# Optimization experiments

Hardware: AMD Instinct MI355X
Metric: run time of the kernel (lower is better)

Reference implementation:

```python
import jax, jax.numpy as jnp
import numpy as np
import math

C = 256
HEADS = 8
WS1 = (8, 8)
SS1 = (0, 0)
WS2 = (8, 8)
SS2 = (4, 4)
CPB_HIDDEN = 512


def _rel_pos_index(ws):
    coords = np.stack(np.meshgrid(np.arange(ws[0]), np.arange(ws[1]), indexing="ij")).reshape(2, -1)
    rel = (coords[:, :, None] - coords[:, None, :]).transpose(1, 2, 0).astype(np.int64)
    rel[..., 0] += ws[0] - 1
    rel[..., 1] += ws[1] - 1
    rel[..., 0] *= 2 * ws[1] - 1
    return rel.sum(-1).reshape(-1)


def _coords_table(ws):
    ch = np.arange(-(ws[0] - 1), ws[0], dtype=np.float32)
    cw = np.arange(-(ws[1] - 1), ws[1], dtype=np.float32)
    t = np.stack(np.meshgrid(ch, cw, indexing="ij"), axis=-1)
    t[..., 0] /= ws[0] - 1
    t[..., 1] /= ws[1] - 1
    t *= 8.0
    t = np.sign(t) * np.log2(np.abs(t) + 1.0) / 3.0
    return t.reshape(-1, 2)


def _swin_mask(pH, pW, ws, ss):
    # standard swin shifted-window attention mask, [num_windows, N, N]
    m = np.zeros((pH, pW), dtype=np.float32)
    cnt = 0.0
    hs = ((0, pH - ws[0]), (pH - ws[0], pH - ss[0]), (pH - ss[0], pH))
    wl = ((0, pW - ws[1]), (pW - ws[1], pW - ss[1]), (pW - ss[1], pW))
    for h0, h1 in hs:
        for w0, w1 in wl:
            m[h0:h1, w0:w1] = cnt
            cnt += 1.0
    m = m.reshape(pH // ws[0], ws[0], pW // ws[1], ws[1]).transpose(0, 2, 1, 3).reshape(-1, ws[0] * ws[1])
    diff = m[:, None, :] - m[:, :, None]
    return np.where(diff != 0.0, -100.0, 0.0).astype(np.float32)


def _swin_attn_v2(x, qkv_w, qkv_b, proj_w, proj_b, logit_scale, cpb_w1, cpb_b1, cpb_w2, ws, ss, num_heads):
    # torchvision ShiftedWindowAttentionV2 forward (dropout=0, eval)
    B, H, W, Cc = x.shape
    L = qkv_b.shape[0] // 3
    qkv_b = jnp.concatenate([qkv_b[:L], jnp.zeros_like(qkv_b[L:2 * L]), qkv_b[2 * L:]])  # v2 zeroes key bias
    pad_b = (ws[0] - H % ws[0]) % ws[0]
    pad_r = (ws[1] - W % ws[1]) % ws[1]
    x = jnp.pad(x, ((0, 0), (0, pad_b), (0, pad_r), (0, 0)))
    pH, pW = H + pad_b, W + pad_r
    s0 = 0 if ws[0] >= pH else ss[0]
    s1 = 0 if ws[1] >= pW else ss[1]
    shifted = (s0 > 0) or (s1 > 0)
    if shifted:
        x = jnp.roll(x, (-s0, -s1), axis=(1, 2))
    nH, nW = pH // ws[0], pW // ws[1]
    N = ws[0] * ws[1]
    xw = x.reshape(B, nH, ws[0], nW, ws[1], Cc).transpose(0, 1, 3, 2, 4, 5).reshape(B * nH * nW, N, Cc)
    qkv = (xw @ qkv_w.T + qkv_b).reshape(-1, N, 3, num_heads, Cc // num_heads).transpose(2, 0, 3, 1, 4)
    q, k, v = qkv[0], qkv[1], qkv[2]
    qn = q / jnp.maximum(jnp.linalg.norm(q, axis=-1, keepdims=True), 1e-12)
    kn = k / jnp.maximum(jnp.linalg.norm(k, axis=-1, keepdims=True), 1e-12)
    scale = jnp.exp(jnp.minimum(logit_scale, math.log(100.0)))  # [heads,1,1]
    attn = jnp.einsum("bhnd,bhmd->bhnm", qn, kn) * scale[None]
    # continuous relative position bias (v2)
    table = jnp.asarray(_coords_table(ws))
    bias_table = jax.nn.relu(table @ cpb_w1.T + cpb_b1) @ cpb_w2.T
    rpb = bias_table[_rel_pos_index(ws)].reshape(N, N, num_heads).transpose(2, 0, 1)
    attn = attn + 16.0 * jax.nn.sigmoid(rpb)[None]
    if shifted:
        mask = jnp.asarray(_swin_mask(pH, pW, ws, (s0, s1)))  # [nWin, N, N]
        attn = (attn.reshape(B, nH * nW, num_heads, N, N) + mask[None, :, None]).reshape(-1, num_heads, N, N)
    attn = jax.nn.softmax(attn, axis=-1)
    out = jnp.einsum("bhnm,bhmd->bhnd", attn, v).transpose(0, 2, 1, 3).reshape(-1, N, Cc)
    out = out @ proj_w.T + proj_b
    out = out.reshape(B, nH, nW, ws[0], ws[1], Cc).transpose(0, 1, 3, 2, 4, 5).reshape(B, pH, pW, Cc)
    if shifted:
        out = jnp.roll(out, (s0, s1), axis=(1, 2))
    return out[:, :H, :W, :]


def _make_params(keys):
    return {
        "qkv_w": jax.random.normal(keys[0], (3 * C, C), dtype=jnp.float32) * 0.02,
        "qkv_b": jax.random.normal(keys[1], (3 * C,), dtype=jnp.float32) * 0.02,
        "proj_w": jax.random.normal(keys[2], (C, C), dtype=jnp.float32) * 0.02,
        "proj_b": jax.random.normal(keys[3], (C,), dtype=jnp.float32) * 0.02,
        "logit_scale": jnp.full((HEADS, 1, 1), math.log(10.0), dtype=jnp.float32),
        "cpb_w1": jax.random.normal(keys[4], (CPB_HIDDEN, 2), dtype=jnp.float32) * 0.02,
        "cpb_b1": jnp.zeros((CPB_HIDDEN,), dtype=jnp.float32),
        "cpb_w2": jax.random.normal(keys[5], (HEADS, CPB_HIDDEN), dtype=jnp.float32) * 0.02,
    }


def setup_inputs() -> dict:
    key = jax.random.key(0)
    ks = jax.random.split(key, 13)
    d = {"src": jax.random.normal(ks[0], (4, 8, C, 64, 64), dtype=jnp.float32)}
    for pre, off in (("a1", 1), ("a2", 7)):
        for name, val in _make_params(ks[off:off + 6]).items():
            d[pre + "_" + name] = val
    return d


def reference(src, a1_qkv_w, a1_qkv_b, a1_proj_w, a1_proj_b, a1_logit_scale, a1_cpb_w1, a1_cpb_b1, a1_cpb_w2, a2_qkv_w, a2_qkv_b, a2_proj_w, a2_proj_b, a2_logit_scale, a2_cpb_w1, a2_cpb_b1, a2_cpb_w2):
    B, T, Cc, H, W = src.shape
    x = src.reshape(B * T, Cc, H, W).transpose(0, 2, 3, 1)  # [BT,H,W,C]
    x = x + _swin_attn_v2(x, a1_qkv_w, a1_qkv_b, a1_proj_w, a1_proj_b, a1_logit_scale, a1_cpb_w1, a1_cpb_b1, a1_cpb_w2, WS1, SS1, HEADS)
    x = x + _swin_attn_v2(x, a2_qkv_w, a2_qkv_b, a2_proj_w, a2_proj_b, a2_logit_scale, a2_cpb_w1, a2_cpb_b1, a2_cpb_w2, WS2, SS2, HEADS)
    return x.transpose(0, 3, 1, 2).reshape(src.shape)
```

## Files before the change

kernel.cpp:

```cpp
#include <hip/hip_runtime.h>


typedef short bf16x8 __attribute__((ext_vector_type(8)));
typedef float f32x4 __attribute__((ext_vector_type(4)));

__device__ __forceinline__ unsigned short f2bf(float f) {
    union { float f; unsigned int u; } v; v.f = f;
    return (unsigned short)((v.u + 0x7fffu + ((v.u >> 16) & 1u)) >> 16);
}
__device__ __forceinline__ float bf2f(unsigned short b) {
    union { unsigned int u; float f; } v; v.u = ((unsigned int)b) << 16;
    return v.f;
}
__device__ __forceinline__ f32x4 mfma_bf16(bf16x8 a, bf16x8 b, f32x4 c) {
    return __builtin_amdgcn_mfma_f32_16x16x32_bf16(a, b, c, 0, 0, 0);
}

__device__ __forceinline__ int region_of(int wh, int ww, int t) {
    int th = t >> 3, tw = t & 7;
    int rh = (wh == 7) ? ((th < 4) ? 1 : 2) : 0;
    int rw = (ww == 7) ? ((tw < 4) ? 1 : 2) : 0;
    return rh * 3 + rw;
}

__global__ __launch_bounds__(256) void k_setup(
    const float* __restrict__ qkvw1, const float* __restrict__ projw1,
    const float* __restrict__ qkvw2, const float* __restrict__ projw2,
    const float* __restrict__ w1a, const float* __restrict__ b1a, const float* __restrict__ w2a,
    const float* __restrict__ w1b, const float* __restrict__ b1b, const float* __restrict__ w2b,
    unsigned short* __restrict__ qw1, unsigned short* __restrict__ pw1,
    unsigned short* __restrict__ qw2, unsigned short* __restrict__ pw2,
    float* __restrict__ bt1, float* __restrict__ bt2)
{
    int b = blockIdx.x, t = threadIdx.x;
    if (b < 512) {
        int idx = b * 256 + t;
        #pragma unroll
        for (int r = 0; r < 4; r++) {
            int i = idx + r * 131072;
            if (i < 196608)        qw1[i]          = f2bf(qkvw1[i]);
            else if (i < 262144)   pw1[i - 196608] = f2bf(projw1[i - 196608]);
            else if (i < 458752)   qw2[i - 262144] = f2bf(qkvw2[i - 262144]);
            else                   pw2[i - 458752] = f2bf(projw2[i - 458752]);
        }
    } else {
        int a = b - 512;
        const float* w1 = a ? w1b : w1a;
        const float* b1 = a ? b1b : b1a;
        const float* w2 = a ? w2b : w2a;
        float* out = a ? bt2 : bt1;
        int k = t;
        if (k >= 225) return;
        int ih = k / 15, iw = k % 15;
        float v0 = (float)(ih - 7) / 7.0f * 8.0f;
        float v1 = (float)(iw - 7) / 7.0f * 8.0f;
        float t0 = (v0 >= 0.f ? 1.f : -1.f) * log2f(fabsf(v0) + 1.f) / 3.0f;
        float t1 = (v1 >= 0.f ? 1.f : -1.f) * log2f(fabsf(v1) + 1.f) / 3.0f;
        float acc[8] = {0.f, 0.f, 0.f, 0.f, 0.f, 0.f, 0.f, 0.f};
        for (int c = 0; c < 512; c++) {
            float hc = t0 * w1[2 * c] + t1 * w1[2 * c + 1] + b1[c];
            hc = fmaxf(hc, 0.f);
            #pragma unroll
            for (int h = 0; h < 8; h++) acc[h] += hc * w2[h * 512 + c];
        }
        #pragma unroll
        for (int h = 0; h < 8; h++) out[k * 8 + h] = 16.f / (1.f + expf(-acc[h]));
    }
}

__global__ __launch_bounds__(256) void t_in(const float* __restrict__ src, float* __restrict__ dst) {
    __shared__ float tile[32][132];
    int img = blockIdx.z, hw0 = blockIdx.x * 128, c0 = blockIdx.y * 32;
    int tid = threadIdx.x;
    #pragma unroll
    for (int k = 0; k < 4; k++) {
        int cl = (tid >> 5) + k * 8;
        int hw4 = (tid & 31) * 4;
        float4 v = *(const float4*)(src + ((size_t)img * 256 + c0 + cl) * 4096 + hw0 + hw4);
        *(float4*)&tile[cl][hw4] = v;
    }
    __syncthreads();
    #pragma unroll
    for (int j = 0; j < 4; j++) {
        int hwl = (tid >> 3) + j * 32;
        int c4 = (tid & 7) * 4;
        float4 o;
        o.x = tile[c4 + 0][hwl]; o.y = tile[c4 + 1][hwl];
        o.z = tile[c4 + 2][hwl]; o.w = tile[c4 + 3][hwl];
        *(float4*)(dst + ((size_t)img * 4096 + hw0 + hwl) * 256 + c0 + c4) = o;
    }
}

__global__ __launch_bounds__(256) void t_out(const float* __restrict__ src, float* __restrict__ dst) {
    __shared__ float tile[32][132];
    int img = blockIdx.z, hw0 = blockIdx.x * 128, c0 = blockIdx.y * 32;
    int tid = threadIdx.x;
    #pragma unroll
    for (int j = 0; j < 4; j++) {
        int hwl = (tid >> 3) + j * 32;
        int c4 = (tid & 7) * 4;
        float4 v = *(const float4*)(src + ((size_t)img * 4096 + hw0 + hwl) * 256 + c0 + c4);
        tile[c4 + 0][hwl] = v.x; tile[c4 + 1][hwl] = v.y;
        tile[c4 + 2][hwl] = v.z; tile[c4 + 3][hwl] = v.w;
    }
    __syncthreads();
    #pragma unroll
    for (int k = 0; k < 4; k++) {
        int cl = (tid >> 5) + k * 8;
        int hw4 = (tid & 31) * 4;
        float4 o = *(const float4*)&tile[cl][hw4];
        *(float4*)(dst + ((size_t)img * 256 + c0 + cl) * 4096 + hw0 + hw4) = o;
    }
}

__global__ __launch_bounds__(256, 2) void k_swin(
    const float* __restrict__ Xin,
    const unsigned short* __restrict__ Wq,
    const float* __restrict__ bq,
    const float* __restrict__ lsc,
    const float* __restrict__ btab,
    const unsigned short* __restrict__ Wp,
    const float* __restrict__ bp,
    unsigned short* __restrict__ AO,
    float* __restrict__ Xout,
    int shift, int masked)
{
    __shared__ __align__(16) unsigned short sX[64 * 264];
    __shared__ __align__(16) unsigned short sQKV[64 * 136];
    __shared__ __align__(16) unsigned short sP[64 * 72];
    __shared__ __align__(16) unsigned short sVt[64 * 72];
    __shared__ float sInv[4 * 64];
    __shared__ float sBias[8 * 225];

    const int tid = threadIdx.x;
    const int wv = tid >> 6, lane = tid & 63, quad = lane >> 4, nn = lane & 15;
    const int win = blockIdx.x;
    const int bt = win >> 6, wh = (win >> 3) & 7, ww = win & 7;
    const f32x4 zero4 = {0.f, 0.f, 0.f, 0.f};

    for (int i = tid; i < 1800; i += 256) {
        int h = i / 225, rel = i - h * 225;
        sBias[i] = btab[rel * 8 + h];
    }

    {
        int tok = tid >> 2, part = tid & 3;
        int h = (wh * 8 + (tok >> 3) + shift) & 63;
        int w = (ww * 8 + (tok & 7) + shift) & 63;
        const float* srcp = Xin + ((size_t)(bt * 4096 + h * 64 + w)) * 256 + part * 64;
        unsigned short* dstp = sX + tok * 264 + part * 64;
        #pragma unroll
        for (int c = 0; c < 64; c += 8) {
            float4 v0 = *(const float4*)(srcp + c);
            float4 v1 = *(const float4*)(srcp + c + 4);
            uint4 o;
            o.x = (unsigned int)f2bf(v0.x) | ((unsigned int)f2bf(v0.y) << 16);
            o.y = (unsigned int)f2bf(v0.z) | ((unsigned int)f2bf(v0.w) << 16);
            o.z = (unsigned int)f2bf(v1.x) | ((unsigned int)f2bf(v1.y) << 16);
            o.w = (unsigned int)f2bf(v1.z) | ((unsigned int)f2bf(v1.w) << 16);
            *(uint4*)(dstp + c) = o;
        }
    }
    __syncthreads();

    int reloff[4][4];
    float madd[4][4];
    #pragma unroll
    for (int ct = 0; ct < 4; ct++) {
        int j = ct * 16 + nn;
        int rj = region_of(wh, ww, j);
        #pragma unroll
        for (int r = 0; r < 4; r++) {
            int i = wv * 16 + quad * 4 + r;
            reloff[ct][r] = ((i >> 3) - (j >> 3) + 7) * 15 + ((i & 7) - (j & 7) + 7);
            madd[ct][r] = (masked && (region_of(wh, ww, i) != rj)) ? -100.f : 0.f;
        }
    }

    const int kind = wv >> 1;
    const int hsel = wv & 1;
    const int vc = wv * 16 + nn;

    for (int p = 0; p < 4; p++) {
        f32x4 acc[4][3];
        #pragma unroll
        for (int rt = 0; rt < 4; rt++)
            #pragma unroll
            for (int c = 0; c < 3; c++) acc[rt][c] = zero4;

        int wrow[3];
        wrow[0] = kind * 256 + (2 * p + hsel) * 32 + nn;
        wrow[1] = wrow[0] + 16;
        wrow[2] = 512 + (2 * p + (vc >> 5)) * 32 + (vc & 31);

        #pragma unroll
        for (int ks = 0; ks < 8; ks++) {
            bf16x8 a[4], b[3];
            #pragma unroll
            for (int rt = 0; rt < 4; rt++)
                a[rt] = *(const bf16x8*)(sX + (rt * 16 + nn) * 264 + ks * 32 + quad * 8);
            #pragma unroll
            for (int c = 0; c < 3; c++)
                b[c] = *(const bf16x8*)(Wq + (size_t)wrow[c] * 256 + ks * 32 + quad * 8);
            #pragma unroll
            for (int rt = 0; rt < 4; rt++)
                #pragma unroll
                for (int c = 0; c < 3; c++)
                    acc[rt][c] = mfma_bf16(a[rt], b[c], acc[rt][c]);
        }

        float ssq[4][4];
        #pragma unroll
        for (int rt = 0; rt < 4; rt++)
            #pragma unroll
            for (int r = 0; r < 4; r++) ssq[rt][r] = 0.f;

        #pragma unroll
        for (int ctl = 0; ctl < 2; ctl++) {
            float bias = kind ? 0.f : bq[wrow[ctl]];
            int col = wv * 32 + ctl * 16 + nn;
            #pragma unroll
            for (int rt = 0; rt < 4; rt++)
                #pragma unroll
                for (int r = 0; r < 4; r++) {
                    float val = acc[rt][ctl][r] + bias;
                    ssq[rt][r] += val * val;
                    sQKV[(rt * 16 + quad * 4 + r) * 136 + col] = f2bf(val);
                }
        }
        {
            float bv = bq[wrow[2]];
            #pragma unroll
            for (int rt = 0; rt < 4; rt++) {
                ushort4 pk;
                pk.x = f2bf(acc[rt][2][0] + bv);
                pk.y = f2bf(acc[rt][2][1] + bv);
                pk.z = f2bf(acc[rt][2][2] + bv);
                pk.w = f2bf(acc[rt][2][3] + bv);
                *(ushort4*)(sVt + vc * 72 + rt * 16 + quad * 4) = pk;
            }
        }
        #pragma unroll
        for (int rt = 0; rt < 4; rt++)
            #pragma unroll
            for (int r = 0; r < 4; r++) {
                float s = ssq[rt][r];
                s += __shfl_xor(s, 1);
                s += __shfl_xor(s, 2);
                s += __shfl_xor(s, 4);
                s += __shfl_xor(s, 8);
                if (nn == 0)
                    sInv[wv * 64 + rt * 16 + quad * 4 + r] = 1.f / fmaxf(sqrtf(s), 1e-12f);
            }
        __syncthreads();

        #pragma unroll
        for (int hh = 0; hh < 2; hh++) {
            const int head = 2 * p + hh;
            const float scale = __expf(fminf(lsc[head], 4.605170185988092f));
            const float* bh = sBias + head * 225;

            bf16x8 aq = *(const bf16x8*)(sQKV + (wv * 16 + nn) * 136 + hh * 32 + quad * 8);
            f32x4 S[4];
            #pragma unroll
            for (int ct = 0; ct < 4; ct++) {
                bf16x8 bk = *(const bf16x8*)(sQKV + (ct * 16 + nn) * 136 + 64 + hh * 32 + quad * 8);
                S[ct] = mfma_bf16(aq, bk, zero4);
            }

            const int i_base = wv * 16 + quad * 4;
            float iq[4];
            #pragma unroll
            for (int r = 0; r < 4; r++) iq[r] = sInv[hh * 64 + i_base + r];

            float rowm[4] = {-3.0e38f, -3.0e38f, -3.0e38f, -3.0e38f};
            #pragma unroll
            for (int ct = 0; ct < 4; ct++) {
                int j = ct * 16 + nn;
                float ivk = sInv[(2 + hh) * 64 + j];
                #pragma unroll
                for (int r = 0; r < 4; r++) {
                    float v = S[ct][r] * iq[r] * ivk * scale + bh[reloff[ct][r]] + madd[ct][r];
                    S[ct][r] = v;
                    rowm[r] = fmaxf(rowm[r], v);
                }
            }
            #pragma unroll
            for (int r = 0; r < 4; r++) {
                float m = rowm[r];
                m = fmaxf(m, __shfl_xor(m, 1));
                m = fmaxf(m, __shfl_xor(m, 2));
                m = fmaxf(m, __shfl_xor(m, 4));
                m = fmaxf(m, __shfl_xor(m, 8));
                rowm[r] = m;
            }
            float rsum[4] = {0.f, 0.f, 0.f, 0.f};
            #pragma unroll
            for (int ct = 0; ct < 4; ct++)
                #pragma unroll
                for (int r = 0; r < 4; r++) {
                    float e = __expf(S[ct][r] - rowm[r]);
                    S[ct][r] = e;
                    rsum[r] += e;
                }
            #pragma unroll
            for (int r = 0; r < 4; r++) {
                float s = rsum[r];
                s += __shfl_xor(s, 1);
                s += __shfl_xor(s, 2);
                s += __shfl_xor(s, 4);
                s += __shfl_xor(s, 8);
                rsum[r] = 1.f / s;
            }
            #pragma unroll
            for (int ct = 0; ct < 4; ct++)
                #pragma unroll
                for (int r = 0; r < 4; r++)
                    sP[(i_base + r) * 72 + ct * 16 + nn] = f2bf(S[ct][r] * rsum[r]);

            bf16x8 ap0 = *(const bf16x8*)(sP + (wv * 16 + nn) * 72 + quad * 8);
            bf16x8 ap1 = *(const bf16x8*)(sP + (wv * 16 + nn) * 72 + 32 + quad * 8);
            #pragma unroll
            for (int ct2 = 0; ct2 < 2; ct2++) {
                bf16x8 bv0 = *(const bf16x8*)(sVt + (hh * 32 + ct2 * 16 + nn) * 72 + quad * 8);
                bf16x8 bv1 = *(const bf16x8*)(sVt + (hh * 32 + ct2 * 16 + nn) * 72 + 32 + quad * 8);
                f32x4 O = mfma_bf16(ap0, bv0, zero4);
                O = mfma_bf16(ap1, bv1, O);
                #pragma unroll
                for (int r = 0; r < 4; r++) {
                    int tokr = i_base + r;
                    AO[((size_t)win * 64 + tokr) * 256 + head * 32 + ct2 * 16 + nn] = f2bf(O[r]);
                }
            }
        }
        __syncthreads();
    }

    {
        int tok = tid >> 2, part = tid & 3;
        const unsigned short* srcp = AO + ((size_t)win * 64 + tok) * 256 + part * 64;
        unsigned short* dstp = sX + tok * 264 + part * 64;
        #pragma unroll
        for (int c = 0; c < 64; c += 8)
            *(uint4*)(dstp + c) = *(const uint4*)(srcp + c);
    }
    __syncthreads();

    f32x4 pacc[4][4];
    #pragma unroll
    for (int rt = 0; rt < 4; rt++)
        #pragma unroll
        for (int c = 0; c < 4; c++) pacc[rt][c] = zero4;

    int prow[4];
    #pragma unroll
    for (int c = 0; c < 4; c++) prow[c] = (wv * 4 + c) * 16 + nn;

    #pragma unroll
    for (int ks = 0; ks < 8; ks++) {
        bf16x8 a[4], b[4];
        #pragma unroll
        for (int rt = 0; rt < 4; rt++)
            a[rt] = *(const bf16x8*)(sX + (rt * 16 + nn) * 264 + ks * 32 + quad * 8);
        #pragma unroll
        for (int c = 0; c < 4; c++)
            b[c] = *(const bf16x8*)(Wp + (size_t)prow[c] * 256 + ks * 32 + quad * 8);
        #pragma unroll
        for (int rt = 0; rt < 4; rt++)
            #pragma unroll
            for (int c = 0; c < 4; c++)
                pacc[rt][c] = mfma_bf16(a[rt], b[c], pacc[rt][c]);
    }

    #pragma unroll
    for (int c = 0; c < 4; c++) {
        int chan = prow[c];
        float bias = bp[chan];
        #pragma unroll
        for (int rt = 0; rt < 4; rt++)
            #pragma unroll
            for (int r = 0; r < 4; r++) {
                int tok = rt * 16 + quad * 4 + r;
                int h = (wh * 8 + (tok >> 3) + shift) & 63;
                int w = (ww * 8 + (tok & 7) + shift) & 63;
                size_t idx = ((size_t)(bt * 4096 + h * 64 + w)) * 256 + chan;
                Xout[idx] = pacc[rt][c][r] + bias + Xin[idx];
            }
    }
}

extern "C" void kernel_launch(void* const* d_in, const int* in_sizes, int n_in,
                              void* d_out, int out_size, void* d_ws, size_t ws_size,
                              hipStream_t stream) {
    (void)in_sizes; (void)n_in; (void)out_size; (void)ws_size;

    const float* src        = (const float*)d_in[0];
    const float* a1_qkv_w   = (const float*)d_in[1];
    const float* a1_qkv_b   = (const float*)d_in[2];
    const float* a1_proj_w  = (const float*)d_in[3];
    const float* a1_proj_b  = (const float*)d_in[4];
    const float* a1_ls      = (const float*)d_in[5];
    const float* a1_w1      = (const float*)d_in[6];
    const float* a1_b1      = (const float*)d_in[7];
    const float* a1_w2      = (const float*)d_in[8];
    const float* a2_qkv_w   = (const float*)d_in[9];
    const float* a2_qkv_b   = (const float*)d_in[10];
    const float* a2_proj_w  = (const float*)d_in[11];
    const float* a2_proj_b  = (const float*)d_in[12];
    const float* a2_ls      = (const float*)d_in[13];
    const float* a2_w1      = (const float*)d_in[14];
    const float* a2_b1      = (const float*)d_in[15];
    const float* a2_w2      = (const float*)d_in[16];

    char* ws = (char*)d_ws;
    const size_t SZ_X = 134217728;
    float* X0 = (float*)(ws);
    float* X1 = (float*)(ws + SZ_X);
    unsigned short* AO  = (unsigned short*)(ws + 2 * SZ_X);
    unsigned short* qw1 = (unsigned short*)(ws + 2 * SZ_X + 67108864);
    unsigned short* qw2 = qw1 + 196608;
    unsigned short* pw1 = qw2 + 196608;
    unsigned short* pw2 = pw1 + 65536;
    float* bt1 = (float*)(pw2 + 65536);
    float* bt2 = bt1 + 1800;

    k_setup<<<514, 256, 0, stream>>>(a1_qkv_w, a1_proj_w, a2_qkv_w, a2_proj_w,
                                     a1_w1, a1_b1, a1_w2, a2_w1, a2_b1, a2_w2,
                                     qw1, pw1, qw2, pw2, bt1, bt2);
    t_in<<<dim3(32, 8, 32), 256, 0, stream>>>(src, X0);

    k_swin<<<2048, 256, 0, stream>>>(X0, qw1, a1_qkv_b, a1_ls, bt1, pw1, a1_proj_b, AO, X1, 0, 0);
    k_swin<<<2048, 256, 0, stream>>>(X1, qw2, a2_qkv_b, a2_ls, bt2, pw2, a2_proj_b, AO, X0, 4, 1);

    t_out<<<dim3(32, 8, 32), 256, 0, stream>>>(X0, (float*)d_out);
}
```

Baseline: 978.8 us.

## Feed MFMA directly from bf16 global activations and drop shared staging buffers

The input transpose now writes bf16 activations, and each swin block emits a bf16 copy of its output for the next block. MFMA A-operands are loaded directly from global memory instead of being staged in a shared sX tile, and the shared bias table is replaced by a global table with a precomputed masked variant. Dropping this shared memory allows raising launch bounds to 4 blocks per SM. The QKV work split across waves and the norm computation are also reorganized, and the first block reads its residual from NCHW src. The costs are uncoalesced global A loads, extra bf16 writes, and a bf16-rounded sum of squares for the norms.

Result: slower. 1.673 ms (+70.9%).

```diff
diff --git a/kernel.cpp b/kernel.cpp
--- a/kernel.cpp
+++ b/kernel.cpp
@@ -64,11 +64,15 @@
             for (int h = 0; h < 8; h++) acc[h] += hc * w2[h * 512 + c];
         }
         #pragma unroll
-        for (int h = 0; h < 8; h++) out[k * 8 + h] = 16.f / (1.f + expf(-acc[h]));
-    }
-}
-
-__global__ __launch_bounds__(256) void t_in(const float* __restrict__ src, float* __restrict__ dst) {
+        for (int h = 0; h < 8; h++) {
+            float s = 16.f / (1.f + expf(-acc[h]));
+            out[k * 8 + h] = s;
+            out[1800 + k * 8 + h] = s - 100.f;
+        }
+    }
+}
+
+__global__ __launch_bounds__(256) void t_in(const float* __restrict__ src, unsigned short* __restrict__ dst) {
     __shared__ float tile[32][132];
     int img = blockIdx.z, hw0 = blockIdx.x * 128, c0 = blockIdx.y * 32;
     int tid = threadIdx.x;
@@ -84,10 +88,10 @@
     for (int j = 0; j < 4; j++) {
         int hwl = (tid >> 3) + j * 32;
         int c4 = (tid & 7) * 4;
-        float4 o;
-        o.x = tile[c4 + 0][hwl]; o.y = tile[c4 + 1][hwl];
-        o.z = tile[c4 + 2][hwl]; o.w = tile[c4 + 3][hwl];
-        *(float4*)(dst + ((size_t)img * 4096 + hw0 + hwl) * 256 + c0 + c4) = o;
+        ushort4 o;
+        o.x = f2bf(tile[c4 + 0][hwl]); o.y = f2bf(tile[c4 + 1][hwl]);
+        o.z = f2bf(tile[c4 + 2][hwl]); o.w = f2bf(tile[c4 + 3][hwl]);
+        *(ushort4*)(dst + ((size_t)img * 4096 + hw0 + hwl) * 256 + c0 + c4) = o;
     }
 }
 
@@ -113,8 +117,9 @@
     }
 }
 
-__global__ __launch_bounds__(256, 2) void k_swin(
-    const float* __restrict__ Xin,
+__global__ __launch_bounds__(256, 4) void k_swin(
+    const float* Xres,
+    const unsigned short* __restrict__ X16,
     const unsigned short* __restrict__ Wq,
     const float* __restrict__ bq,
     const float* __restrict__ lsc,
@@ -122,15 +127,14 @@
     const unsigned short* __restrict__ Wp,
     const float* __restrict__ bp,
     unsigned short* __restrict__ AO,
-    float* __restrict__ Xout,
-    int shift, int masked)
+    float* Xout,
+    unsigned short* __restrict__ Xout16,
+    int shift, int masked, int res_nchw)
 {
-    __shared__ __align__(16) unsigned short sX[64 * 264];
     __shared__ __align__(16) unsigned short sQKV[64 * 136];
     __shared__ __align__(16) unsigned short sP[64 * 72];
     __shared__ __align__(16) unsigned short sVt[64 * 72];
-    __shared__ float sInv[4 * 64];
-    __shared__ float sBias[8 * 225];
+    __shared__ float sInv[256];
 
     const int tid = threadIdx.x;
     const int wv = tid >> 6, lane = tid & 63, quad = lane >> 4, nn = lane & 15;
@@ -138,33 +142,16 @@
     const int bt = win >> 6, wh = (win >> 3) & 7, ww = win & 7;
     const f32x4 zero4 = {0.f, 0.f, 0.f, 0.f};
 
-    for (int i = tid; i < 1800; i += 256) {
-        int h = i / 225, rel = i - h * 225;
-        sBias[i] = btab[rel * 8 + h];
-    }
-
-    {
-        int tok = tid >> 2, part = tid & 3;
+    size_t abase[4];
+    #pragma unroll
+    for (int rt = 0; rt < 4; rt++) {
+        int tok = rt * 16 + nn;
         int h = (wh * 8 + (tok >> 3) + shift) & 63;
         int w = (ww * 8 + (tok & 7) + shift) & 63;
-        const float* srcp = Xin + ((size_t)(bt * 4096 + h * 64 + w)) * 256 + part * 64;
-        unsigned short* dstp = sX + tok * 264 + part * 64;
-        #pragma unroll
-        for (int c = 0; c < 64; c += 8) {
-            float4 v0 = *(const float4*)(srcp + c);
-            float4 v1 = *(const float4*)(srcp + c + 4);
-            uint4 o;
-            o.x = (unsigned int)f2bf(v0.x) | ((unsigned int)f2bf(v0.y) << 16);
-            o.y = (unsigned int)f2bf(v0.z) | ((unsigned int)f2bf(v0.w) << 16);
-            o.z = (unsigned int)f2bf(v1.x) | ((unsigned int)f2bf(v1.y) << 16);
-            o.w = (unsigned int)f2bf(v1.z) | ((unsigned int)f2bf(v1.w) << 16);
-            *(uint4*)(dstp + c) = o;
-        }
-    }
-    __syncthreads();
+        abase[rt] = ((size_t)(bt * 4096 + h * 64 + w)) * 256;
+    }
 
     int reloff[4][4];
-    float madd[4][4];
     #pragma unroll
     for (int ct = 0; ct < 4; ct++) {
         int j = ct * 16 + nn;
@@ -172,14 +159,11 @@
         #pragma unroll
         for (int r = 0; r < 4; r++) {
             int i = wv * 16 + quad * 4 + r;
-            reloff[ct][r] = ((i >> 3) - (j >> 3) + 7) * 15 + ((i & 7) - (j & 7) + 7);
-            madd[ct][r] = (masked && (region_of(wh, ww, i) != rj)) ? -100.f : 0.f;
-        }
-    }
-
-    const int kind = wv >> 1;
-    const int hsel = wv & 1;
-    const int vc = wv * 16 + nn;
+            int rel = ((i >> 3) - (j >> 3) + 7) * 15 + ((i & 7) - (j & 7) + 7);
+            bool mk = masked && (region_of(wh, ww, i) != rj);
+            reloff[ct][r] = rel * 8 + (mk ? 1800 : 0);
+        }
+    }
 
     for (int p = 0; p < 4; p++) {
         f32x4 acc[4][3];
@@ -188,17 +172,24 @@
             #pragma unroll
             for (int c = 0; c < 3; c++) acc[rt][c] = zero4;
 
-        int wrow[3];
-        wrow[0] = kind * 256 + (2 * p + hsel) * 32 + nn;
-        wrow[1] = wrow[0] + 16;
-        wrow[2] = 512 + (2 * p + (vc >> 5)) * 32 + (vc & 31);
-
+        int wrow[3], secv[3], colb[3];
+        #pragma unroll
+        for (int c = 0; c < 3; c++) {
+            int ct = wv * 3 + c;
+            int sec = ct >> 1;
+            int kind = sec >> 1;
+            int head = 2 * p + (sec & 1);
+            wrow[c] = kind * 256 + head * 32 + (ct & 1) * 16 + nn;
+            secv[c] = sec;
+            colb[c] = (sec < 4) ? (sec * 32 + (ct & 1) * 16 + nn)
+                                : ((sec - 4) * 32 + (ct & 1) * 16 + nn);
+        }
         #pragma unroll
         for (int ks = 0; ks < 8; ks++) {
             bf16x8 a[4], b[3];
             #pragma unroll
             for (int rt = 0; rt < 4; rt++)
-                a[rt] = *(const bf16x8*)(sX + (rt * 16 + nn) * 264 + ks * 32 + quad * 8);
+                a[rt] = *(const bf16x8*)(X16 + abase[rt] + ks * 32 + quad * 8);
             #pragma unroll
             for (int c = 0; c < 3; c++)
                 b[c] = *(const bf16x8*)(Wq + (size_t)wrow[c] * 256 + ks * 32 + quad * 8);
@@ -209,56 +200,50 @@
                     acc[rt][c] = mfma_bf16(a[rt], b[c], acc[rt][c]);
         }
 
-        float ssq[4][4];
-        #pragma unroll
-        for (int rt = 0; rt < 4; rt++)
-            #pragma unroll
-            for (int r = 0; r < 4; r++) ssq[rt][r] = 0.f;
-
-        #pragma unroll
-        for (int ctl = 0; ctl < 2; ctl++) {
-            float bias = kind ? 0.f : bq[wrow[ctl]];
-            int col = wv * 32 + ctl * 16 + nn;
-            #pragma unroll
-            for (int rt = 0; rt < 4; rt++)
-                #pragma unroll
-                for (int r = 0; r < 4; r++) {
-                    float val = acc[rt][ctl][r] + bias;
-                    ssq[rt][r] += val * val;
-                    sQKV[(rt * 16 + quad * 4 + r) * 136 + col] = f2bf(val);
+        #pragma unroll
+        for (int c = 0; c < 3; c++) {
+            int sec = secv[c];
+            if (sec < 4) {
+                float bias = (sec >= 2) ? 0.f : bq[wrow[c]];
+                int col = colb[c];
+                #pragma unroll
+                for (int rt = 0; rt < 4; rt++)
+                    #pragma unroll
+                    for (int r = 0; r < 4; r++)
+                        sQKV[(rt * 16 + quad * 4 + r) * 136 + col] = f2bf(acc[rt][c][r] + bias);
+            } else {
+                float bv = bq[wrow[c]];
+                int vchan = colb[c];
+                #pragma unroll
+                for (int rt = 0; rt < 4; rt++)
+                    #pragma unroll
+                    for (int r = 0; r < 4; r++)
+                        sVt[vchan * 72 + rt * 16 + quad * 4 + r] = f2bf(acc[rt][c][r] + bv);
+            }
+        }
+        __syncthreads();
+
+        {
+            int t = tid & 63, sec = tid >> 6;
+            const unsigned short* row = sQKV + t * 136 + sec * 32;
+            float ss = 0.f;
+            #pragma unroll
+            for (int j = 0; j < 4; j++) {
+                bf16x8 v = *(const bf16x8*)(row + j * 8);
+                #pragma unroll
+                for (int i = 0; i < 8; i++) {
+                    float f = bf2f((unsigned short)v[i]);
+                    ss += f * f;
                 }
-        }
-        {
-            float bv = bq[wrow[2]];
-            #pragma unroll
-            for (int rt = 0; rt < 4; rt++) {
-                ushort4 pk;
-                pk.x = f2bf(acc[rt][2][0] + bv);
-                pk.y = f2bf(acc[rt][2][1] + bv);
-                pk.z = f2bf(acc[rt][2][2] + bv);
-                pk.w = f2bf(acc[rt][2][3] + bv);
-                *(ushort4*)(sVt + vc * 72 + rt * 16 + quad * 4) = pk;
-            }
-        }
-        #pragma unroll
-        for (int rt = 0; rt < 4; rt++)
-            #pragma unroll
-            for (int r = 0; r < 4; r++) {
-                float s = ssq[rt][r];
-                s += __shfl_xor(s, 1);
-                s += __shfl_xor(s, 2);
-                s += __shfl_xor(s, 4);
-                s += __shfl_xor(s, 8);
-                if (nn == 0)
-                    sInv[wv * 64 + rt * 16 + quad * 4 + r] = 1.f / fmaxf(sqrtf(s), 1e-12f);
-            }
+            }
+            sInv[sec * 64 + t] = 1.f / fmaxf(sqrtf(ss), 1e-12f);
+        }
         __syncthreads();
 
         #pragma unroll
         for (int hh = 0; hh < 2; hh++) {
             const int head = 2 * p + hh;
             const float scale = __expf(fminf(lsc[head], 4.605170185988092f));
-            const float* bh = sBias + head * 225;
 
             bf16x8 aq = *(const bf16x8*)(sQKV + (wv * 16 + nn) * 136 + hh * 32 + quad * 8);
             f32x4 S[4];
@@ -280,7 +265,7 @@
                 float ivk = sInv[(2 + hh) * 64 + j];
                 #pragma unroll
                 for (int r = 0; r < 4; r++) {
-                    float v = S[ct][r] * iq[r] * ivk * scale + bh[reloff[ct][r]] + madd[ct][r];
+                    float v = S[ct][r] * iq[r] * ivk * scale + btab[reloff[ct][r] + head];
                     S[ct][r] = v;
                     rowm[r] = fmaxf(rowm[r], v);
                 }
@@ -336,16 +321,6 @@
         __syncthreads();
     }
 
-    {
-        int tok = tid >> 2, part = tid & 3;
-        const unsigned short* srcp = AO + ((size_t)win * 64 + tok) * 256 + part * 64;
-        unsigned short* dstp = sX + tok * 264 + part * 64;
-        #pragma unroll
-        for (int c = 0; c < 64; c += 8)
-            *(uint4*)(dstp + c) = *(const uint4*)(srcp + c);
-    }
-    __syncthreads();
-
     f32x4 pacc[4][4];
     #pragma unroll
     for (int rt = 0; rt < 4; rt++)
@@ -361,7 +336,7 @@
         bf16x8 a[4], b[4];
         #pragma unroll
         for (int rt = 0; rt < 4; rt++)
-            a[rt] = *(const bf16x8*)(sX + (rt * 16 + nn) * 264 + ks * 32 + quad * 8);
+            a[rt] = *(const bf16x8*)(AO + ((size_t)win * 64 + rt * 16 + nn) * 256 + ks * 32 + quad * 8);
         #pragma unroll
         for (int c = 0; c < 4; c++)
             b[c] = *(const bf16x8*)(Wp + (size_t)prow[c] * 256 + ks * 32 + quad * 8);
@@ -384,7 +359,11 @@
                 int h = (wh * 8 + (tok >> 3) + shift) & 63;
                 int w = (ww * 8 + (tok & 7) + shift) & 63;
                 size_t idx = ((size_t)(bt * 4096 + h * 64 + w)) * 256 + chan;
-                Xout[idx] = pacc[rt][c][r] + bias + Xin[idx];
+                float res = res_nchw ? Xres[((size_t)(bt * 256 + chan)) * 4096 + h * 64 + w]
+                                     : Xres[idx];
+                float o = pacc[rt][c][r] + bias + res;
+                Xout[idx] = o;
+                if (Xout16) Xout16[idx] = f2bf(o);
             }
     }
 }
@@ -413,24 +392,26 @@
     const float* a2_w2      = (const float*)d_in[16];
 
     char* ws = (char*)d_ws;
-    const size_t SZ_X = 134217728;
-    float* X0 = (float*)(ws);
-    float* X1 = (float*)(ws + SZ_X);
-    unsigned short* AO  = (unsigned short*)(ws + 2 * SZ_X);
-    unsigned short* qw1 = (unsigned short*)(ws + 2 * SZ_X + 67108864);
+    float* X1           = (float*)(ws);
+    unsigned short* X0b = (unsigned short*)(ws + 134217728);
+    unsigned short* X1b = (unsigned short*)(ws + 201326592);
+    unsigned short* AO  = (unsigned short*)(ws + 268435456);
+    unsigned short* qw1 = (unsigned short*)(ws + 335544320);
     unsigned short* qw2 = qw1 + 196608;
     unsigned short* pw1 = qw2 + 196608;
     unsigned short* pw2 = pw1 + 65536;
     float* bt1 = (float*)(pw2 + 65536);
-    float* bt2 = bt1 + 1800;
+    float* bt2 = bt1 + 3600;
 
     k_setup<<<514, 256, 0, stream>>>(a1_qkv_w, a1_proj_w, a2_qkv_w, a2_proj_w,
                                      a1_w1, a1_b1, a1_w2, a2_w1, a2_b1, a2_w2,
                                      qw1, pw1, qw2, pw2, bt1, bt2);
-    t_in<<<dim3(32, 8, 32), 256, 0, stream>>>(src, X0);
-
-    k_swin<<<2048, 256, 0, stream>>>(X0, qw1, a1_qkv_b, a1_ls, bt1, pw1, a1_proj_b, AO, X1, 0, 0);
-    k_swin<<<2048, 256, 0, stream>>>(X1, qw2, a2_qkv_b, a2_ls, bt2, pw2, a2_proj_b, AO, X0, 4, 1);
-
-    t_out<<<dim3(32, 8, 32), 256, 0, stream>>>(X0, (float*)d_out);
-}
+    t_in<<<dim3(32, 8, 32), 256, 0, stream>>>(src, X0b);
+
+    k_swin<<<2048, 256, 0, stream>>>(src, X0b, qw1, a1_qkv_b, a1_ls, bt1,
+                                     pw1, a1_proj_b, AO, X1, X1b, 0, 0, 1);
+    k_swin<<<2048, 256, 0, stream>>>(X1, X1b, qw2, a2_qkv_b, a2_ls, bt2,
+                                     pw2, a2_proj_b, AO, X1, (unsigned short*)nullptr, 4, 1, 0);
+
+    t_out<<<dim3(32, 8, 32), 256, 0, stream>>>(X1, (float*)d_out);
+}
```
